# Optimization experiments

Hardware: AMD Instinct MI355X
Metric: run time of the kernel (lower is better)

The kernel has to match this reference:

```python
import jax, jax.numpy as jnp
import numpy as np

N, E, G = 10000, 160000, 64      # nodes, edges, graphs
IN, H, L = 128, 128, 14          # in_channels, hidden, num GENConv layers
EPS_LN = 1e-5                    # torch LayerNorm eps
EPS_MSG = 1e-7                   # GENConv message eps


def layer_norm(x, g, b):
    mu = jnp.mean(x, axis=-1, keepdims=True)
    v = jnp.var(x, axis=-1, keepdims=True)
    return (x - mu) * jax.lax.rsqrt(v + EPS_LN) * g + b


def gen_conv(h, src, dst, t, sc, W1, b1, mg, mb, W2, b2):
    # message: relu(x_j) + eps  (no edge_attr)
    msg = jax.nn.relu(h[src]) + EPS_MSG                      # [E, H]
    # softmax aggregation over edges sharing a destination, per feature
    z = msg * t
    mx = jax.ops.segment_max(z, dst, num_segments=N)         # [N, H]
    mx = jnp.where(jnp.isfinite(mx), mx, 0.0)
    e = jnp.exp(z - mx[dst])
    ssum = jax.ops.segment_sum(e, dst, num_segments=N)
    alpha = e / (ssum[dst] + 1e-16)
    agg = jax.ops.segment_sum(msg * alpha, dst, num_segments=N)  # [N, H]
    # MessageNorm: normalize(agg) * ||h|| * scale
    agg = agg / jnp.maximum(jnp.linalg.norm(agg, axis=-1, keepdims=True), 1e-12)
    agg = agg * jnp.linalg.norm(h, axis=-1, keepdims=True) * sc
    out = h + agg
    # MLP [H, 2H, H] with LayerNorm + ReLU between (dropout off in eval)
    z1 = layer_norm(out @ W1 + b1, mg, mb)
    return jax.nn.relu(z1) @ W2 + b2


def setup_inputs() -> dict:
    key = jax.random.key(0)
    ks = jax.random.split(key, 8)
    s = 0.05
    x = jax.random.normal(ks[0], (N, IN), jnp.float32)
    edge_index = jax.random.randint(ks[1], (2, E), 0, N, dtype=jnp.int64)
    batch = jnp.sort(jax.random.randint(ks[2], (N,), 0, G, dtype=jnp.int64))
    enc_W = jax.random.normal(ks[3], (IN, H), jnp.float32) * s
    enc_b = jnp.zeros((H,), jnp.float32)
    ln_g = jnp.ones((L, H), jnp.float32)
    ln_b = jnp.zeros((L, H), jnp.float32)
    t = jnp.ones((L,), jnp.float32)         # learnable softmax temperature
    scale = jnp.ones((L,), jnp.float32)     # learnable MsgNorm scale
    W1 = jax.random.normal(ks[4], (L, H, 2 * H), jnp.float32) * s
    b1 = jnp.zeros((L, 2 * H), jnp.float32)
    mg = jnp.ones((L, 2 * H), jnp.float32)
    mb = jnp.zeros((L, 2 * H), jnp.float32)
    W2 = jax.random.normal(ks[5], (L, 2 * H, H), jnp.float32) * s
    b2 = jnp.zeros((L, H), jnp.float32)
    fn_g = jnp.ones((H,), jnp.float32)
    fn_b = jnp.zeros((H,), jnp.float32)
    return dict(x=x, edge_index=edge_index, batch=batch, enc_W=enc_W, enc_b=enc_b,
                ln_g=ln_g, ln_b=ln_b, t=t, scale=scale, W1=W1, b1=b1, mg=mg, mb=mb,
                W2=W2, b2=b2, fn_g=fn_g, fn_b=fn_b)


def reference(x, edge_index, batch, enc_W, enc_b, ln_g, ln_b, t, scale,
              W1, b1, mg, mb, W2, b2, fn_g, fn_b):
    src, dst = edge_index[0], edge_index[1]
    h = x @ enc_W + enc_b
    for i in range(L):  # DeepGCNLayer 'res+': x + conv(act(norm(x)))
        r = jax.nn.leaky_relu(layer_norm(h, ln_g[i], ln_b[i]), 0.01)
        h = h + gen_conv(r, src, dst, t[i], scale[i],
                         W1[i], b1[i], mg[i], mb[i], W2[i], b2[i])
    h = jax.nn.leaky_relu(layer_norm(h, fn_g, fn_b), 0.01)
    # global_mean_pool (fin_map is unused in the original forward)
    cnt = jax.ops.segment_sum(jnp.ones((N,), h.dtype), batch, num_segments=G)
    gf = jax.ops.segment_sum(h, batch, num_segments=G) / jnp.maximum(cnt, 1.0)[:, None]
    return gf
```

## Files before the change

### kernel.cpp

```cpp
#include <hip/hip_runtime.h>
#include <cstdint>
#include <cstddef>


#define BT 512

typedef __attribute__((ext_vector_type(8))) short bf16x8;
typedef __attribute__((ext_vector_type(4))) float f32x4;

__device__ inline float bf2f(ushort u) {
    union { uint i; float f; } v;
    v.i = (uint)u << 16;
    return v.f;
}
__device__ inline ushort f2bf(float f) {
    union { float f; uint i; } v;
    v.f = f;
    return (ushort)((v.i + 0x7fffu + ((v.i >> 16) & 1u)) >> 16);
}
__device__ inline uint f2bf2(float a, float b) {
    return (uint)f2bf(a) | ((uint)f2bf(b) << 16);
}
__device__ inline float fast_exp2(float x) {
    return __builtin_amdgcn_exp2f(x);
}

__global__ void setup_kernel(const float* __restrict__ x, ushort* __restrict__ xb,
                             const int* __restrict__ dst, int* __restrict__ deg,
                             const int* __restrict__ batch, int* __restrict__ gstart,
                             int total, int N, int E, int G) {
    int idx = blockIdx.x * blockDim.x + threadIdx.x;
    if (idx >= total) return;
    xb[idx] = f2bf(x[idx]);
    if (idx < E) atomicAdd(&deg[dst[idx]], 1);
    if (idx < N) {
        int bb = batch[idx];
        if (idx == 0)
            for (int g = 0; g <= bb; g++) gstart[g] = 0;
        else {
            int pb = batch[idx - 1];
            for (int g = pb + 1; g <= bb; g++) gstart[g] = idx;
        }
        if (idx == N - 1)
            for (int g = bb + 1; g <= G; g++) gstart[g] = N;
    }
}

__global__ __launch_bounds__(1024) void scan_kernel(const int* __restrict__ deg,
                                                    int* __restrict__ offs,
                                                    int* __restrict__ cursor, int N) {
    __shared__ int part[1024];
    int tid = threadIdx.x;
    int CH = (N + 1023) / 1024;
    int base = tid * CH;
    int s = 0;
    for (int i = 0; i < CH; i++) {
        int idx = base + i;
        if (idx < N) s += deg[idx];
    }
    part[tid] = s;
    __syncthreads();
    for (int off = 1; off < 1024; off <<= 1) {
        int v = (tid >= off) ? part[tid - off] : 0;
        __syncthreads();
        part[tid] += v;
        __syncthreads();
    }
    int run = (tid == 0) ? 0 : part[tid - 1];
    for (int i = 0; i < CH; i++) {
        int idx = base + i;
        if (idx < N) {
            offs[idx] = run;
            cursor[idx] = run;
            run += deg[idx];
        }
    }
    if (tid == 1023) offs[N] = part[1023];
}

__global__ void scatter_kernel(const int* __restrict__ src, const int* __restrict__ dst,
                               int* __restrict__ cursor, int* __restrict__ esrc, int E) {
    int e = blockIdx.x * blockDim.x + threadIdx.x;
    if (e < E) {
        int d = dst[e];
        int pos = atomicAdd(&cursor[d], 1);
        esrc[pos] = src[e];
    }
}

__global__ __launch_bounds__(1024) void sort_kernel(const int* __restrict__ offs,
                                                    int* __restrict__ perm, int N) {
    __shared__ int hist[256];
    __shared__ int cur[256];
    int tid = threadIdx.x;
    if (tid < 256) hist[tid] = 0;
    __syncthreads();
    for (int n = tid; n < N; n += 1024) {
        int d = offs[n + 1] - offs[n];
        int key = 255 - min(d, 255);
        atomicAdd(&hist[key], 1);
    }
    __syncthreads();
    if (tid == 0) {
        int run = 0;
        for (int i = 0; i < 256; i++) {
            cur[i] = run;
            run += hist[i];
        }
    }
    __syncthreads();
    for (int n = tid; n < N; n += 1024) {
        int d = offs[n + 1] - offs[n];
        int key = 255 - min(d, 255);
        int pos = atomicAdd(&cur[key], 1);
        perm[pos] = n;
    }
}

__global__ __launch_bounds__(256) void prep_kernel(const float* __restrict__ W1,
                                                   const float* __restrict__ W2,
                                                   const float* __restrict__ encW,
                                                   ushort* __restrict__ W1t,
                                                   ushort* __restrict__ W2t,
                                                   ushort* __restrict__ encWt, int L) {
    __shared__ float tile[32][33];
    int z = blockIdx.z;
    const float* in;
    ushort* out;
    int R, C;
    if (z < L) {
        in = W1 + (size_t)z * 32768; out = W1t + (size_t)z * 32768; R = 128; C = 256;
    } else if (z < 2 * L) {
        int i = z - L;
        in = W2 + (size_t)i * 32768; out = W2t + (size_t)i * 32768; R = 256; C = 128;
    } else {
        in = encW; out = encWt; R = 128; C = 128;
    }
    int r0 = blockIdx.y * 32, c0 = blockIdx.x * 32;
    if (r0 >= R || c0 >= C) return;
    int tx = threadIdx.x & 31, ty = threadIdx.x >> 5;
    for (int i = ty; i < 32; i += 8) tile[i][tx] = in[(size_t)(r0 + i) * C + c0 + tx];
    __syncthreads();
    for (int i = ty; i < 32; i += 8)
        out[(size_t)(c0 + i) * R + r0 + tx] = f2bf(tile[tx][i]);
}

__device__ __forceinline__ void agg_stage(const ushort* __restrict__ rin,
                                          const int* __restrict__ offs,
                                          const int* __restrict__ esrc,
                                          const float* __restrict__ rnbuf,
                                          float tv2, float sv,
                                          int nd0, int nd1,
                                          int w, int l, uint (*AsU)[68]) {
    const uint2* rin2 = (const uint2*)rin;
    int half = l >> 5, li = l & 31;
    int eb[2], dg[2];
    eb[0] = offs[nd0]; dg[0] = offs[nd0 + 1] - eb[0];
    eb[1] = offs[nd1]; dg[1] = offs[nd1 + 1] - eb[1];

    uint2 ru0 = rin2[(size_t)nd0 * 32 + li];
    uint2 ru1 = rin2[(size_t)nd1 * 32 + li];
    float rn0 = rnbuf[nd0], rn1 = rnbuf[nd1];

    float s[2][4] = {}, W[2][4] = {};
    int mxdeg = max(dg[0], dg[1]);

#pragma unroll 1
    for (int base = 0; base < mxdeg; base += 64) {
        int rem0 = min(dg[0] - base, 64);
        int rem1 = min(dg[1] - base, 64);
        int idx0 = (rem0 > 0 && l < rem0) ? esrc[eb[0] + base + l] : 0;
        int idx1 = (rem1 > 0 && l < rem1) ? esrc[eb[1] + base + l] : 0;
        int it = (max(rem0, rem1) + 7) >> 3;
#pragma unroll 1
        for (int i = 0; i < it; i++) {
            int j0 = i * 8 + half;
            uint2 rv[2][4];
            bool vl[2][4];
#pragma unroll
            for (int c = 0; c < 4; c++) {
                int j = j0 + 2 * c;
                vl[0][c] = j < rem0;
                vl[1][c] = j < rem1;
                int sn0 = __shfl(idx0, j, 64);
                int sn1 = __shfl(idx1, j, 64);
                if (vl[0][c]) rv[0][c] = rin2[(size_t)sn0 * 32 + li];
                if (vl[1][c]) rv[1][c] = rin2[(size_t)sn1 * 32 + li];
            }
#pragma unroll
            for (int k = 0; k < 2; k++)
#pragma unroll
                for (int c = 0; c < 4; c++) {
                    if (vl[k][c]) {
                        float f0 = bf2f((ushort)(rv[k][c].x & 0xffff));
                        float f1 = bf2f((ushort)(rv[k][c].x >> 16));
                        float f2 = bf2f((ushort)(rv[k][c].y & 0xffff));
                        float f3 = bf2f((ushort)(rv[k][c].y >> 16));
                        float g0 = fmaxf(f0, 0.f) + 1e-7f;
                        float g1 = fmaxf(f1, 0.f) + 1e-7f;
                        float g2 = fmaxf(f2, 0.f) + 1e-7f;
                        float g3 = fmaxf(f3, 0.f) + 1e-7f;
                        float p0 = fast_exp2(g0 * tv2);
                        float p1 = fast_exp2(g1 * tv2);
                        float p2 = fast_exp2(g2 * tv2);
                        float p3 = fast_exp2(g3 * tv2);
                        s[k][0] += p0; W[k][0] += g0 * p0;
                        s[k][1] += p1; W[k][1] += g1 * p1;
                        s[k][2] += p2; W[k][2] += g2 * p2;
                        s[k][3] += p3; W[k][3] += g3 * p3;
                    }
                }
        }
    }

#pragma unroll
    for (int k = 0; k < 2; k++) {
#pragma unroll
        for (int f = 0; f < 4; f++) {
            s[k][f] += __shfl_xor(s[k][f], 32, 64);
            W[k][f] += __shfl_xor(W[k][f], 32, 64);
        }
        float agg[4], nsq = 0.f;
#pragma unroll
        for (int f = 0; f < 4; f++) {
            agg[f] = W[k][f] / (s[k][f] + 1e-16f);
            nsq += agg[f] * agg[f];
        }
#pragma unroll
        for (int off = 1; off < 32; off <<= 1) nsq += __shfl_xor(nsq, off, 64);
        float rnv = (k == 0) ? rn0 : rn1;
        uint2 ru = (k == 0) ? ru0 : ru1;
        float fac = rnv * sv / fmaxf(sqrtf(nsq), 1e-12f);
        if (half == 0) {
            uint2 o;
            o.x = f2bf2(bf2f((ushort)(ru.x & 0xffff)) + agg[0] * fac,
                        bf2f((ushort)(ru.x >> 16)) + agg[1] * fac);
            o.y = f2bf2(bf2f((ushort)(ru.y & 0xffff)) + agg[2] * fac,
                        bf2f((ushort)(ru.y >> 16)) + agg[3] * fac);
            *(uint2*)&AsU[2 * w + k][2 * li] = o;
        }
    }
}

__device__ __forceinline__ void gemm1_stage8(const ushort (*As)[136],
                                             const ushort* __restrict__ Bt,
                                             const float* __restrict__ bias,
                                             const float* __restrict__ mg,
                                             const float* __restrict__ mb,
                                             ushort (*z1s)[264],
                                             int w, int q, int ln,
                                             float (*pS)[16], float (*pQ)[16]) {
    f32x4 acc[2];
    acc[0] = (f32x4){0.f, 0.f, 0.f, 0.f};
    acc[1] = (f32x4){0.f, 0.f, 0.f, 0.f};
#pragma unroll
    for (int ks = 0; ks < 128; ks += 32) {
        bf16x8 a = *(const bf16x8*)&As[ln][ks + q * 8];
#pragma unroll
        for (int ct = 0; ct < 2; ct++) {
            bf16x8 bv = *(const bf16x8*)(Bt + (size_t)(w * 32 + ct * 16 + ln) * 128 + ks + q * 8);
            acc[ct] = __builtin_amdgcn_mfma_f32_16x16x32_bf16(a, bv, acc[ct], 0, 0, 0);
        }
    }
    float s1[4] = {0, 0, 0, 0}, s2[4] = {0, 0, 0, 0};
#pragma unroll
    for (int ct = 0; ct < 2; ct++)
#pragma unroll
        for (int r = 0; r < 4; r++) {
            float v = acc[ct][r] + bias[w * 32 + ct * 16 + ln];
            acc[ct][r] = v;
            s1[r] += v;
            s2[r] += v * v;
        }
#pragma unroll
    for (int off = 1; off < 16; off <<= 1)
#pragma unroll
        for (int r = 0; r < 4; r++) {
            s1[r] += __shfl_xor(s1[r], off, 64);
            s2[r] += __shfl_xor(s2[r], off, 64);
        }
    if (ln == 0)
#pragma unroll
        for (int r = 0; r < 4; r++) {
            pS[w][q * 4 + r] = s1[r];
            pQ[w][q * 4 + r] = s2[r];
        }
    __syncthreads();
#pragma unroll
    for (int r = 0; r < 4; r++) {
        int row = q * 4 + r;
        float S = 0.f, Q = 0.f;
#pragma unroll
        for (int ww = 0; ww < 8; ww++) {
            S += pS[ww][row];
            Q += pQ[ww][row];
        }
        float mu = S * (1.f / 256.f);
        float var = Q * (1.f / 256.f) - mu * mu;
        float rs = rsqrtf(var + 1e-5f);
#pragma unroll
        for (int ct = 0; ct < 2; ct++) {
            int col = w * 32 + ct * 16 + ln;
            float y = (acc[ct][r] - mu) * rs * mg[col] + mb[col];
            z1s[row][col] = f2bf(fmaxf(y, 0.f));
        }
    }
    __syncthreads();
}

template <int KD, bool RESID>
__device__ __forceinline__ void out_stage8(const ushort* __restrict__ Abase, int astr,
                                           const ushort* __restrict__ Bt,
                                           const float* __restrict__ bias,
                                           const float* __restrict__ lg,
                                           const float* __restrict__ lb,
                                           ushort* __restrict__ hbuf,
                                           ushort* __restrict__ rout,
                                           float* __restrict__ rnbuf,
                                           const int* rowmap,
                                           int w, int q, int ln,
                                           float (*pS)[16], float (*pQ)[16]) {
    f32x4 acc = (f32x4){0.f, 0.f, 0.f, 0.f};
    int col = w * 16 + ln;
#pragma unroll
    for (int ks = 0; ks < KD; ks += 32) {
        bf16x8 a = *(const bf16x8*)(Abase + ln * astr + ks + q * 8);
        bf16x8 bv = *(const bf16x8*)(Bt + (size_t)col * KD + ks + q * 8);
        acc = __builtin_amdgcn_mfma_f32_16x16x32_bf16(a, bv, acc, 0, 0, 0);
    }
    float s1[4], s2[4];
#pragma unroll
    for (int r = 0; r < 4; r++) {
        int grow = rowmap[q * 4 + r];
        float v = acc[r] + bias[col];
        if (RESID) v += bf2f(__builtin_nontemporal_load(hbuf + (size_t)grow * 128 + col));
        __builtin_nontemporal_store(f2bf(v), hbuf + (size_t)grow * 128 + col);
        acc[r] = v;
        s1[r] = v;
        s2[r] = v * v;
    }
#pragma unroll
    for (int off = 1; off < 16; off <<= 1)
#pragma unroll
        for (int r = 0; r < 4; r++) {
            s1[r] += __shfl_xor(s1[r], off, 64);
            s2[r] += __shfl_xor(s2[r], off, 64);
        }
    if (ln == 0)
#pragma unroll
        for (int r = 0; r < 4; r++) {
            pS[w][q * 4 + r] = s1[r];
            pQ[w][q * 4 + r] = s2[r];
        }
    __syncthreads();
    float yv[4];
    float t2[4];
#pragma unroll
    for (int r = 0; r < 4; r++) {
        int row = q * 4 + r;
        float S = 0.f, Q = 0.f;
#pragma unroll
        for (int ww = 0; ww < 8; ww++) {
            S += pS[ww][row];
            Q += pQ[ww][row];
        }
        float mu = S * (1.f / 128.f);
        float var = Q * (1.f / 128.f) - mu * mu;
        float rs = rsqrtf(var + 1e-5f);
        float y = (acc[r] - mu) * rs * lg[col] + lb[col];
        y = y > 0.f ? y : 0.01f * y;
        yv[r] = y;
        t2[r] = y * y;
    }
#pragma unroll
    for (int off = 1; off < 16; off <<= 1)
#pragma unroll
        for (int r = 0; r < 4; r++) t2[r] += __shfl_xor(t2[r], off, 64);
    __syncthreads();
    if (ln == 0)
#pragma unroll
        for (int r = 0; r < 4; r++) pS[w][q * 4 + r] = t2[r];
    __syncthreads();
#pragma unroll
    for (int r = 0; r < 4; r++) {
        int grow = rowmap[q * 4 + r];
        float T = 0.f;
#pragma unroll
        for (int ww = 0; ww < 8; ww++) T += pS[ww][q * 4 + r];
        if (w == 0 && ln == 0) rnbuf[grow] = sqrtf(T);
        __builtin_nontemporal_store(f2bf(yv[r]), rout + (size_t)grow * 128 + col);
    }
}

__global__ __launch_bounds__(BT, 4) void enc_kernel(const ushort* __restrict__ xb,
                                                    const ushort* __restrict__ encWt,
                                                    const float* __restrict__ encB,
                                                    const float* __restrict__ lg,
                                                    const float* __restrict__ lb,
                                                    ushort* __restrict__ h,
                                                    ushort* __restrict__ rbuf,
                                                    float* __restrict__ rn, int N) {
    __shared__ __align__(16) ushort As[16][136];
    __shared__ float pS[8][16], pQ[8][16];
    __shared__ int rowmap[16];
    uint(*AsU)[68] = (uint(*)[68])As;
    int tid = threadIdx.x, w = tid >> 6, l = tid & 63;
    int q = l >> 4, ln = l & 15;
    int row0 = blockIdx.x * 16;
    if (tid < 16) rowmap[tid] = row0 + tid;
    for (int idx = tid; idx < 16 * 64; idx += BT) {
        int row = idx >> 6, cl = idx & 63;
        AsU[row][cl] =
            __builtin_nontemporal_load(((const uint*)xb) + (size_t)(row0 + row) * 64 + cl);
    }
    __syncthreads();
    out_stage8<128, false>(&As[0][0], 136, encWt, encB, lg, lb, h, rbuf, rn,
                           rowmap, w, q, ln, pS, pQ);
}

__global__ __launch_bounds__(BT, 4) void layer_kernel(const ushort* __restrict__ rin,
                                                      ushort* __restrict__ rout,
                                                      const int* __restrict__ offs,
                                                      const int* __restrict__ esrc,
                                                      const int* __restrict__ perm,
                                                      float* __restrict__ rn,
                                                      ushort* __restrict__ h,
                                                      const ushort* __restrict__ W1t,
                                                      const ushort* __restrict__ W2t,
                                                      const float* __restrict__ b1,
                                                      const float* __restrict__ mg,
                                                      const float* __restrict__ mb,
                                                      const float* __restrict__ b2,
                                                      const float* __restrict__ ng,
                                                      const float* __restrict__ nb,
                                                      const float* __restrict__ tptr,
                                                      const float* __restrict__ scptr,
                                                      int N) {
    __shared__ __align__(16) ushort As[16][136];
    __shared__ __align__(16) ushort z1s[16][264];
    __shared__ float pS[8][16], pQ[8][16];
    __shared__ int rowmap[16];
    uint(*AsU)[68] = (uint(*)[68])As;
    int tid = threadIdx.x, w = tid >> 6, l = tid & 63;
    int q = l >> 4, ln = l & 15;
    int row0 = blockIdx.x * 16;
    if (tid < 16) rowmap[tid] = perm[row0 + tid];
    __syncthreads();
    float tv2 = (*tptr) * 1.4426950408889634f;
    float sv = *scptr;
    agg_stage(rin, offs, esrc, rn, tv2, sv,
              rowmap[2 * w], rowmap[2 * w + 1], w, l, AsU);
    __syncthreads();
    gemm1_stage8(As, W1t, b1, mg, mb, z1s, w, q, ln, pS, pQ);
    out_stage8<256, true>(&z1s[0][0], 264, W2t, b2, ng, nb, h, rout, rn,
                          rowmap, w, q, ln, pS, pQ);
}

__global__ __launch_bounds__(256) void pool_kernel(const ushort* __restrict__ rf,
                                                   const int* __restrict__ gstart,
                                                   float* __restrict__ out) {
    __shared__ float pb0[4][64], pb1[4][64];
    int g = blockIdx.x;
    int w = threadIdx.x >> 6, l = threadIdx.x & 63;
    int s = gstart[g], e = gstart[g + 1];
    float a0 = 0.f, a1 = 0.f;
    for (int n = s + w; n < e; n += 4) {
        uint rv = __builtin_nontemporal_load(((const uint*)rf) + (size_t)n * 64 + l);
        a0 += bf2f((ushort)(rv & 0xffff));
        a1 += bf2f((ushort)(rv >> 16));
    }
    pb0[w][l] = a0;
    pb1[w][l] = a1;
    __syncthreads();
    if (threadIdx.x < 64) {
        float t0 = pb0[0][l] + pb0[1][l] + pb0[2][l] + pb0[3][l];
        float t1 = pb1[0][l] + pb1[1][l] + pb1[2][l] + pb1[3][l];
        float inv = 1.f / fmaxf((float)(e - s), 1.f);
        out[g * 128 + 2 * l] = t0 * inv;
        out[g * 128 + 2 * l + 1] = t1 * inv;
    }
}

extern "C" void kernel_launch(void* const* d_in, const int* in_sizes, int n_in,
                              void* d_out, int out_size, void* d_ws, size_t ws_size,
                              hipStream_t stream) {
    const float* x     = (const float*)d_in[0];
    const int*   ei    = (const int*)d_in[1];
    const int*   batch = (const int*)d_in[2];
    const float* encW  = (const float*)d_in[3];
    const float* encB  = (const float*)d_in[4];
    const float* ln_g  = (const float*)d_in[5];
    const float* ln_b  = (const float*)d_in[6];
    const float* tArr  = (const float*)d_in[7];
    const float* scArr = (const float*)d_in[8];
    const float* W1    = (const float*)d_in[9];
    const float* b1    = (const float*)d_in[10];
    const float* mg    = (const float*)d_in[11];
    const float* mb    = (const float*)d_in[12];
    const float* W2    = (const float*)d_in[13];
    const float* b2    = (const float*)d_in[14];
    const float* fn_g  = (const float*)d_in[15];
    const float* fn_b  = (const float*)d_in[16];
    float* out = (float*)d_out;

    const int N = in_sizes[0] / 128;
    const int E = in_sizes[1] / 2;
    const int L = in_sizes[7];
    const int G = 64;

    const int* src = ei;
    const int* dst = ei + E;

    char* p = (char*)d_ws;
    auto alloc = [&](size_t bytes) -> void* {
        void* qp = (void*)p;
        p += (bytes + 255) & ~(size_t)255;
        return qp;
    };
    int*    deg    = (int*)alloc((size_t)N * 4);
    int*    offs   = (int*)alloc((size_t)(N + 1) * 4);
    int*    cursor = (int*)alloc((size_t)N * 4);
    int*    esrc   = (int*)alloc((size_t)E * 4);
    int*    gstart = (int*)alloc((size_t)(G + 1) * 4);
    int*    perm   = (int*)alloc((size_t)N * 4);
    ushort* h      = (ushort*)alloc((size_t)N * 128 * 2);
    ushort* r0     = (ushort*)alloc((size_t)N * 128 * 2);
    ushort* r1     = (ushort*)alloc((size_t)N * 128 * 2);
    float*  rn     = (float*)alloc((size_t)N * 4);
    ushort* xb     = (ushort*)alloc((size_t)N * 128 * 2);
    ushort* W1t    = (ushort*)alloc((size_t)L * 32768 * 2);
    ushort* W2t    = (ushort*)alloc((size_t)L * 32768 * 2);
    ushort* encWt  = (ushort*)alloc((size_t)16384 * 2);

    (void)hipMemsetAsync(deg, 0, (size_t)N * 4, stream);

    setup_kernel<<<(N * 128 + 255) / 256, 256, 0, stream>>>(x, xb, dst, deg, batch,
                                                            gstart, N * 128, N, E, G);
    scan_kernel<<<1, 1024, 0, stream>>>(deg, offs, cursor, N);
    scatter_kernel<<<(E + 255) / 256, 256, 0, stream>>>(src, dst, cursor, esrc, E);
    sort_kernel<<<1, 1024, 0, stream>>>(offs, perm, N);
    prep_kernel<<<dim3(8, 8, 2 * L + 1), 256, 0, stream>>>(W1, W2, encW, W1t, W2t,
                                                           encWt, L);

    const int TILES = N / 16;

    enc_kernel<<<TILES, BT, 0, stream>>>(xb, encWt, encB, ln_g, ln_b, h, r0, rn, N);

    for (int i = 0; i < L; i++) {
        const ushort* rin = (i & 1) ? r1 : r0;
        ushort* rout = (i & 1) ? r0 : r1;
        const float* ng = (i < L - 1) ? (ln_g + (size_t)(i + 1) * 128) : fn_g;
        const float* nb = (i < L - 1) ? (ln_b + (size_t)(i + 1) * 128) : fn_b;
        layer_kernel<<<TILES, BT, 0, stream>>>(rin, rout, offs, esrc, perm, rn, h,
                                               W1t + ((size_t)i << 15),
                                               W2t + ((size_t)i << 15),
                                               b1 + (size_t)i * 256,
                                               mg + (size_t)i * 256,
                                               mb + (size_t)i * 256,
                                               b2 + (size_t)i * 128,
                                               ng, nb, tArr + i, scArr + i, N);
    }

    const ushort* rf = ((L - 1) & 1) ? r0 : r1;
    pool_kernel<<<G, 256, 0, stream>>>(rf, gstart, out);
}
```

Baseline: 572.4 us.

## Fuse encoder, all layers and pooling into one persistent kernel with grid barriers

```diff
diff --git a/kernel.cpp b/kernel.cpp
--- a/kernel.cpp
+++ b/kernel.cpp
@@ -4,6 +4,7 @@
 
 
 #define BT 512
+#define NBLK 512
 
 typedef __attribute__((ext_vector_type(8))) short bf16x8;
 typedef __attribute__((ext_vector_type(4))) float f32x4;
@@ -23,6 +24,23 @@
 }
 __device__ inline float fast_exp2(float x) {
     return __builtin_amdgcn_exp2f(x);
+}
+
+__device__ __forceinline__ void gbar(uint* __restrict__ bar, uint nb) {
+    __syncthreads();
+    if (threadIdx.x == 0) {
+        uint g = __hip_atomic_load(bar + 1, __ATOMIC_RELAXED, __HIP_MEMORY_SCOPE_AGENT);
+        uint v = __hip_atomic_fetch_add(bar + 0, 1u, __ATOMIC_ACQ_REL, __HIP_MEMORY_SCOPE_AGENT);
+        if (v == nb - 1u) {
+            __hip_atomic_store(bar + 0, 0u, __ATOMIC_RELAXED, __HIP_MEMORY_SCOPE_AGENT);
+            __hip_atomic_fetch_add(bar + 1, 1u, __ATOMIC_RELEASE, __HIP_MEMORY_SCOPE_AGENT);
+        } else {
+            while (__hip_atomic_load(bar + 1, __ATOMIC_RELAXED, __HIP_MEMORY_SCOPE_AGENT) == g)
+                __builtin_amdgcn_s_sleep(4);
+            __threadfence();
+        }
+    }
+    __syncthreads();
 }
 
 __global__ void setup_kernel(const float* __restrict__ x, ushort* __restrict__ xb,
@@ -392,50 +410,33 @@
     }
 }
 
-__global__ __launch_bounds__(BT, 4) void enc_kernel(const ushort* __restrict__ xb,
-                                                    const ushort* __restrict__ encWt,
-                                                    const float* __restrict__ encB,
-                                                    const float* __restrict__ lg,
-                                                    const float* __restrict__ lb,
-                                                    ushort* __restrict__ h,
-                                                    ushort* __restrict__ rbuf,
-                                                    float* __restrict__ rn, int N) {
-    __shared__ __align__(16) ushort As[16][136];
-    __shared__ float pS[8][16], pQ[8][16];
-    __shared__ int rowmap[16];
-    uint(*AsU)[68] = (uint(*)[68])As;
-    int tid = threadIdx.x, w = tid >> 6, l = tid & 63;
-    int q = l >> 4, ln = l & 15;
-    int row0 = blockIdx.x * 16;
-    if (tid < 16) rowmap[tid] = row0 + tid;
-    for (int idx = tid; idx < 16 * 64; idx += BT) {
-        int row = idx >> 6, cl = idx & 63;
-        AsU[row][cl] =
-            __builtin_nontemporal_load(((const uint*)xb) + (size_t)(row0 + row) * 64 + cl);
-    }
-    __syncthreads();
-    out_stage8<128, false>(&As[0][0], 136, encWt, encB, lg, lb, h, rbuf, rn,
-                           rowmap, w, q, ln, pS, pQ);
-}
-
-__global__ __launch_bounds__(BT, 4) void layer_kernel(const ushort* __restrict__ rin,
-                                                      ushort* __restrict__ rout,
-                                                      const int* __restrict__ offs,
-                                                      const int* __restrict__ esrc,
-                                                      const int* __restrict__ perm,
-                                                      float* __restrict__ rn,
-                                                      ushort* __restrict__ h,
-                                                      const ushort* __restrict__ W1t,
-                                                      const ushort* __restrict__ W2t,
-                                                      const float* __restrict__ b1,
-                                                      const float* __restrict__ mg,
-                                                      const float* __restrict__ mb,
-                                                      const float* __restrict__ b2,
-                                                      const float* __restrict__ ng,
-                                                      const float* __restrict__ nb,
-                                                      const float* __restrict__ tptr,
-                                                      const float* __restrict__ scptr,
-                                                      int N) {
+__global__ __launch_bounds__(BT, 4) void fused_kernel(
+    const ushort* __restrict__ xb,
+    const ushort* __restrict__ encWt,
+    const float* __restrict__ encB,
+    const float* __restrict__ ln_g,
+    const float* __restrict__ ln_b,
+    const float* __restrict__ fn_g,
+    const float* __restrict__ fn_b,
+    const float* __restrict__ tArr,
+    const float* __restrict__ scArr,
+    const ushort* __restrict__ W1t,
+    const ushort* __restrict__ W2t,
+    const float* __restrict__ b1,
+    const float* __restrict__ mg,
+    const float* __restrict__ mb,
+    const float* __restrict__ b2,
+    const int* __restrict__ offs,
+    const int* __restrict__ esrc,
+    const int* __restrict__ perm,
+    float* __restrict__ rn,
+    ushort* __restrict__ h,
+    ushort* __restrict__ r0,
+    ushort* __restrict__ r1,
+    const int* __restrict__ gstart,
+    float* __restrict__ out,
+    uint* __restrict__ bar,
+    int N, int L, int G) {
     __shared__ __align__(16) ushort As[16][136];
     __shared__ __align__(16) ushort z1s[16][264];
     __shared__ float pS[8][16], pQ[8][16];
@@ -443,41 +444,95 @@
     uint(*AsU)[68] = (uint(*)[68])As;
     int tid = threadIdx.x, w = tid >> 6, l = tid & 63;
     int q = l >> 4, ln = l & 15;
-    int row0 = blockIdx.x * 16;
-    if (tid < 16) rowmap[tid] = perm[row0 + tid];
-    __syncthreads();
-    float tv2 = (*tptr) * 1.4426950408889634f;
-    float sv = *scptr;
-    agg_stage(rin, offs, esrc, rn, tv2, sv,
-              rowmap[2 * w], rowmap[2 * w + 1], w, l, AsU);
-    __syncthreads();
-    gemm1_stage8(As, W1t, b1, mg, mb, z1s, w, q, ln, pS, pQ);
-    out_stage8<256, true>(&z1s[0][0], 264, W2t, b2, ng, nb, h, rout, rn,
-                          rowmap, w, q, ln, pS, pQ);
-}
-
-__global__ __launch_bounds__(256) void pool_kernel(const ushort* __restrict__ rf,
-                                                   const int* __restrict__ gstart,
-                                                   float* __restrict__ out) {
-    __shared__ float pb0[4][64], pb1[4][64];
-    int g = blockIdx.x;
-    int w = threadIdx.x >> 6, l = threadIdx.x & 63;
-    int s = gstart[g], e = gstart[g + 1];
-    float a0 = 0.f, a1 = 0.f;
-    for (int n = s + w; n < e; n += 4) {
-        uint rv = __builtin_nontemporal_load(((const uint*)rf) + (size_t)n * 64 + l);
-        a0 += bf2f((ushort)(rv & 0xffff));
-        a1 += bf2f((ushort)(rv >> 16));
-    }
-    pb0[w][l] = a0;
-    pb1[w][l] = a1;
-    __syncthreads();
-    if (threadIdx.x < 64) {
-        float t0 = pb0[0][l] + pb0[1][l] + pb0[2][l] + pb0[3][l];
-        float t1 = pb1[0][l] + pb1[1][l] + pb1[2][l] + pb1[3][l];
-        float inv = 1.f / fmaxf((float)(e - s), 1.f);
-        out[g * 128 + 2 * l] = t0 * inv;
-        out[g * 128 + 2 * l + 1] = t1 * inv;
+    int bid = blockIdx.x;
+    const int NB = (int)gridDim.x;
+    const int TILES = N / 16;
+
+    int singles = 2 * NB - TILES;
+    int t0, t1;
+    if (bid < singles) {
+        t0 = bid; t1 = -1;
+    } else {
+        int k = bid - singles;
+        t0 = singles + 2 * k;
+        t1 = t0 + 1;
+    }
+    if (t0 >= TILES) t0 = -1;
+    if (t1 >= TILES) t1 = -1;
+
+    for (int ii = 0; ii < 2; ii++) {
+        int t = ii ? t1 : t0;
+        if (t < 0) continue;
+        int row0 = t * 16;
+        if (tid < 16) rowmap[tid] = row0 + tid;
+        for (int idx = tid; idx < 16 * 64; idx += BT) {
+            int rr = idx >> 6, cl = idx & 63;
+            AsU[rr][cl] = __builtin_nontemporal_load(
+                ((const uint*)xb) + (size_t)(row0 + rr) * 64 + cl);
+        }
+        __syncthreads();
+        out_stage8<128, false>(&As[0][0], 136, encWt, encB, ln_g, ln_b, h, r0, rn,
+                               rowmap, w, q, ln, pS, pQ);
+        __syncthreads();
+    }
+    gbar(bar, (uint)NB);
+
+    for (int i = 0; i < L; i++) {
+        const ushort* rin = (i & 1) ? r1 : r0;
+        ushort* rout = (i & 1) ? r0 : r1;
+        const float* ng = (i < L - 1) ? (ln_g + (size_t)(i + 1) * 128) : fn_g;
+        const float* nbv = (i < L - 1) ? (ln_b + (size_t)(i + 1) * 128) : fn_b;
+        const ushort* w1 = W1t + ((size_t)i << 15);
+        const ushort* w2 = W2t + ((size_t)i << 15);
+        const float* b1i = b1 + (size_t)i * 256;
+        const float* mgi = mg + (size_t)i * 256;
+        const float* mbi = mb + (size_t)i * 256;
+        const float* b2i = b2 + (size_t)i * 128;
+        float tv2 = tArr[i] * 1.4426950408889634f;
+        float sv = scArr[i];
+        for (int ii = 0; ii < 2; ii++) {
+            int t = ii ? t1 : t0;
+            if (t < 0) continue;
+            int row0 = t * 16;
+            if (tid < 16) rowmap[tid] = perm[row0 + tid];
+            __syncthreads();
+            agg_stage(rin, offs, esrc, rn, tv2, sv,
+                      rowmap[2 * w], rowmap[2 * w + 1], w, l, AsU);
+            __syncthreads();
+            gemm1_stage8(As, w1, b1i, mgi, mbi, z1s, w, q, ln, pS, pQ);
+            out_stage8<256, true>(&z1s[0][0], 264, w2, b2i, ng, nbv, h, rout, rn,
+                                  rowmap, w, q, ln, pS, pQ);
+            __syncthreads();
+        }
+        gbar(bar, (uint)NB);
+    }
+
+    if (bid < G) {
+        const ushort* rf = ((L - 1) & 1) ? r0 : r1;
+        float* pb0 = (float*)&z1s[0][0];
+        float* pb1 = pb0 + 8 * 64;
+        int g = bid;
+        int s = gstart[g], e = gstart[g + 1];
+        float a0 = 0.f, a1 = 0.f;
+        for (int n = s + w; n < e; n += 8) {
+            uint rv = ((const uint*)rf)[(size_t)n * 64 + l];
+            a0 += bf2f((ushort)(rv & 0xffff));
+            a1 += bf2f((ushort)(rv >> 16));
+        }
+        pb0[w * 64 + l] = a0;
+        pb1[w * 64 + l] = a1;
+        __syncthreads();
+        if (tid < 64) {
+            float s0 = 0.f, s1 = 0.f;
+#pragma unroll
+            for (int ww = 0; ww < 8; ww++) {
+                s0 += pb0[ww * 64 + tid];
+                s1 += pb1[ww * 64 + tid];
+            }
+            float inv = 1.f / fmaxf((float)(e - s), 1.f);
+            out[g * 128 + 2 * tid] = s0 * inv;
+            out[g * 128 + 2 * tid + 1] = s1 * inv;
+        }
     }
 }
 
@@ -531,8 +586,10 @@
     ushort* W1t    = (ushort*)alloc((size_t)L * 32768 * 2);
     ushort* W2t    = (ushort*)alloc((size_t)L * 32768 * 2);
     ushort* encWt  = (ushort*)alloc((size_t)16384 * 2);
+    uint*   bar    = (uint*)alloc(256);
 
     (void)hipMemsetAsync(deg, 0, (size_t)N * 4, stream);
+    (void)hipMemsetAsync(bar, 0, 256, stream);
 
     setup_kernel<<<(N * 128 + 255) / 256, 256, 0, stream>>>(x, xb, dst, deg, batch,
                                                             gstart, N * 128, N, E, G);
@@ -542,25 +599,8 @@
     prep_kernel<<<dim3(8, 8, 2 * L + 1), 256, 0, stream>>>(W1, W2, encW, W1t, W2t,
                                                            encWt, L);
 
-    const int TILES = N / 16;
-
-    enc_kernel<<<TILES, BT, 0, stream>>>(xb, encWt, encB, ln_g, ln_b, h, r0, rn, N);
-
-    for (int i = 0; i < L; i++) {
-        const ushort* rin = (i & 1) ? r1 : r0;
-        ushort* rout = (i & 1) ? r0 : r1;
-        const float* ng = (i < L - 1) ? (ln_g + (size_t)(i + 1) * 128) : fn_g;
-        const float* nb = (i < L - 1) ? (ln_b + (size_t)(i + 1) * 128) : fn_b;
-        layer_kernel<<<TILES, BT, 0, stream>>>(rin, rout, offs, esrc, perm, rn, h,
-                                               W1t + ((size_t)i << 15),
-                                               W2t + ((size_t)i << 15),
-                                               b1 + (size_t)i * 256,
-                                               mg + (size_t)i * 256,
-                                               mb + (size_t)i * 256,
-                                               b2 + (size_t)i * 128,
-                                               ng, nb, tArr + i, scArr + i, N);
-    }
-
-    const ushort* rf = ((L - 1) & 1) ? r0 : r1;
-    pool_kernel<<<G, 256, 0, stream>>>(rf, gstart, out);
-}
+    fused_kernel<<<NBLK, BT, 0, stream>>>(xb, encWt, encB, ln_g, ln_b, fn_g, fn_b,
+                                          tArr, scArr, W1t, W2t, b1, mg, mb, b2,
+                                          offs, esrc, perm, rn, h, r0, r1,
+                                          gstart, out, bar, N, L, G);
+}
```

Result: slower. 1.643 ms (+187.1%).

## Halve block size to 256 threads and process 8 rows per block

Applied to the files above, without the earlier changes.

```diff
diff --git a/kernel.cpp b/kernel.cpp
--- a/kernel.cpp
+++ b/kernel.cpp
@@ -3,7 +3,7 @@
 #include <cstddef>
 
 
-#define BT 512
+#define BT 256
 
 typedef __attribute__((ext_vector_type(8))) short bf16x8;
 typedef __attribute__((ext_vector_type(4))) float f32x4;
@@ -242,7 +242,7 @@
     }
 }
 
-__device__ __forceinline__ void gemm1_stage8(const ushort (*As)[136],
+__device__ __forceinline__ void gemm1_stage4(const ushort (*As)[136],
                                              const ushort* __restrict__ Bt,
                                              const float* __restrict__ bias,
                                              const float* __restrict__ mg,
@@ -250,24 +250,24 @@
                                              ushort (*z1s)[264],
                                              int w, int q, int ln,
                                              float (*pS)[16], float (*pQ)[16]) {
-    f32x4 acc[2];
-    acc[0] = (f32x4){0.f, 0.f, 0.f, 0.f};
-    acc[1] = (f32x4){0.f, 0.f, 0.f, 0.f};
+    f32x4 acc[4];
+#pragma unroll
+    for (int ct = 0; ct < 4; ct++) acc[ct] = (f32x4){0.f, 0.f, 0.f, 0.f};
 #pragma unroll
     for (int ks = 0; ks < 128; ks += 32) {
         bf16x8 a = *(const bf16x8*)&As[ln][ks + q * 8];
 #pragma unroll
-        for (int ct = 0; ct < 2; ct++) {
-            bf16x8 bv = *(const bf16x8*)(Bt + (size_t)(w * 32 + ct * 16 + ln) * 128 + ks + q * 8);
+        for (int ct = 0; ct < 4; ct++) {
+            bf16x8 bv = *(const bf16x8*)(Bt + (size_t)(w * 64 + ct * 16 + ln) * 128 + ks + q * 8);
             acc[ct] = __builtin_amdgcn_mfma_f32_16x16x32_bf16(a, bv, acc[ct], 0, 0, 0);
         }
     }
     float s1[4] = {0, 0, 0, 0}, s2[4] = {0, 0, 0, 0};
 #pragma unroll
-    for (int ct = 0; ct < 2; ct++)
+    for (int ct = 0; ct < 4; ct++)
 #pragma unroll
         for (int r = 0; r < 4; r++) {
-            float v = acc[ct][r] + bias[w * 32 + ct * 16 + ln];
+            float v = acc[ct][r] + bias[w * 64 + ct * 16 + ln];
             acc[ct][r] = v;
             s1[r] += v;
             s2[r] += v * v;
@@ -291,7 +291,7 @@
         int row = q * 4 + r;
         float S = 0.f, Q = 0.f;
 #pragma unroll
-        for (int ww = 0; ww < 8; ww++) {
+        for (int ww = 0; ww < 4; ww++) {
             S += pS[ww][row];
             Q += pQ[ww][row];
         }
@@ -299,8 +299,8 @@
         float var = Q * (1.f / 256.f) - mu * mu;
         float rs = rsqrtf(var + 1e-5f);
 #pragma unroll
-        for (int ct = 0; ct < 2; ct++) {
-            int col = w * 32 + ct * 16 + ln;
+        for (int ct = 0; ct < 4; ct++) {
+            int col = w * 64 + ct * 16 + ln;
             float y = (acc[ct][r] - mu) * rs * mg[col] + mb[col];
             z1s[row][col] = f2bf(fmaxf(y, 0.f));
         }
@@ -309,7 +309,7 @@
 }
 
 template <int KD, bool RESID>
-__device__ __forceinline__ void out_stage8(const ushort* __restrict__ Abase, int astr,
+__device__ __forceinline__ void out_stage4(const ushort* __restrict__ Abase, int astr,
                                            const ushort* __restrict__ Bt,
                                            const float* __restrict__ bias,
                                            const float* __restrict__ lg,
@@ -320,24 +320,36 @@
                                            const int* rowmap,
                                            int w, int q, int ln,
                                            float (*pS)[16], float (*pQ)[16]) {
-    f32x4 acc = (f32x4){0.f, 0.f, 0.f, 0.f};
-    int col = w * 16 + ln;
+    f32x4 acc[2];
+    acc[0] = (f32x4){0.f, 0.f, 0.f, 0.f};
+    acc[1] = (f32x4){0.f, 0.f, 0.f, 0.f};
+    int col0 = w * 32 + ln;
+    int col1 = w * 32 + 16 + ln;
 #pragma unroll
     for (int ks = 0; ks < KD; ks += 32) {
         bf16x8 a = *(const bf16x8*)(Abase + ln * astr + ks + q * 8);
-        bf16x8 bv = *(const bf16x8*)(Bt + (size_t)col * KD + ks + q * 8);
-        acc = __builtin_amdgcn_mfma_f32_16x16x32_bf16(a, bv, acc, 0, 0, 0);
-    }
-    float s1[4], s2[4];
+        bf16x8 b0 = *(const bf16x8*)(Bt + (size_t)col0 * KD + ks + q * 8);
+        bf16x8 b1v = *(const bf16x8*)(Bt + (size_t)col1 * KD + ks + q * 8);
+        acc[0] = __builtin_amdgcn_mfma_f32_16x16x32_bf16(a, b0, acc[0], 0, 0, 0);
+        acc[1] = __builtin_amdgcn_mfma_f32_16x16x32_bf16(a, b1v, acc[1], 0, 0, 0);
+    }
+    float v0[4], v1[4], s1[4], s2[4];
 #pragma unroll
     for (int r = 0; r < 4; r++) {
-        int grow = rowmap[q * 4 + r];
-        float v = acc[r] + bias[col];
-        if (RESID) v += bf2f(__builtin_nontemporal_load(hbuf + (size_t)grow * 128 + col));
-        __builtin_nontemporal_store(f2bf(v), hbuf + (size_t)grow * 128 + col);
-        acc[r] = v;
-        s1[r] = v;
-        s2[r] = v * v;
+        int row = q * 4 + r;
+        int grow = rowmap[row];
+        v0[r] = acc[0][r] + bias[col0];
+        v1[r] = acc[1][r] + bias[col1];
+        if (row < 8) {
+            if (RESID) {
+                v0[r] += bf2f(__builtin_nontemporal_load(hbuf + (size_t)grow * 128 + col0));
+                v1[r] += bf2f(__builtin_nontemporal_load(hbuf + (size_t)grow * 128 + col1));
+            }
+            __builtin_nontemporal_store(f2bf(v0[r]), hbuf + (size_t)grow * 128 + col0);
+            __builtin_nontemporal_store(f2bf(v1[r]), hbuf + (size_t)grow * 128 + col1);
+        }
+        s1[r] = v0[r] + v1[r];
+        s2[r] = v0[r] * v0[r] + v1[r] * v1[r];
     }
 #pragma unroll
     for (int off = 1; off < 16; off <<= 1)
@@ -353,24 +365,26 @@
             pQ[w][q * 4 + r] = s2[r];
         }
     __syncthreads();
-    float yv[4];
-    float t2[4];
+    float y0[4], y1[4], t2[4];
 #pragma unroll
     for (int r = 0; r < 4; r++) {
         int row = q * 4 + r;
         float S = 0.f, Q = 0.f;
 #pragma unroll
-        for (int ww = 0; ww < 8; ww++) {
+        for (int ww = 0; ww < 4; ww++) {
             S += pS[ww][row];
             Q += pQ[ww][row];
         }
         float mu = S * (1.f / 128.f);
         float var = Q * (1.f / 128.f) - mu * mu;
         float rs = rsqrtf(var + 1e-5f);
-        float y = (acc[r] - mu) * rs * lg[col] + lb[col];
-        y = y > 0.f ? y : 0.01f * y;
-        yv[r] = y;
-        t2[r] = y * y;
+        float a0 = (v0[r] - mu) * rs * lg[col0] + lb[col0];
+        float a1 = (v1[r] - mu) * rs * lg[col1] + lb[col1];
+        a0 = a0 > 0.f ? a0 : 0.01f * a0;
+        a1 = a1 > 0.f ? a1 : 0.01f * a1;
+        y0[r] = a0;
+        y1[r] = a1;
+        t2[r] = a0 * a0 + a1 * a1;
     }
 #pragma unroll
     for (int off = 1; off < 16; off <<= 1)
@@ -383,16 +397,20 @@
     __syncthreads();
 #pragma unroll
     for (int r = 0; r < 4; r++) {
-        int grow = rowmap[q * 4 + r];
-        float T = 0.f;
-#pragma unroll
-        for (int ww = 0; ww < 8; ww++) T += pS[ww][q * 4 + r];
-        if (w == 0 && ln == 0) rnbuf[grow] = sqrtf(T);
-        __builtin_nontemporal_store(f2bf(yv[r]), rout + (size_t)grow * 128 + col);
-    }
-}
-
-__global__ __launch_bounds__(BT, 4) void enc_kernel(const ushort* __restrict__ xb,
+        int row = q * 4 + r;
+        if (row < 8) {
+            int grow = rowmap[row];
+            float T = 0.f;
+#pragma unroll
+            for (int ww = 0; ww < 4; ww++) T += pS[ww][row];
+            if (w == 0 && ln == 0) rnbuf[grow] = sqrtf(T);
+            __builtin_nontemporal_store(f2bf(y0[r]), rout + (size_t)grow * 128 + col0);
+            __builtin_nontemporal_store(f2bf(y1[r]), rout + (size_t)grow * 128 + col1);
+        }
+    }
+}
+
+__global__ __launch_bounds__(BT, 6) void enc_kernel(const ushort* __restrict__ xb,
                                                     const ushort* __restrict__ encWt,
                                                     const float* __restrict__ encB,
                                                     const float* __restrict__ lg,
@@ -401,24 +419,24 @@
                                                     ushort* __restrict__ rbuf,
                                                     float* __restrict__ rn, int N) {
     __shared__ __align__(16) ushort As[16][136];
-    __shared__ float pS[8][16], pQ[8][16];
+    __shared__ float pS[4][16], pQ[4][16];
     __shared__ int rowmap[16];
     uint(*AsU)[68] = (uint(*)[68])As;
     int tid = threadIdx.x, w = tid >> 6, l = tid & 63;
     int q = l >> 4, ln = l & 15;
-    int row0 = blockIdx.x * 16;
-    if (tid < 16) rowmap[tid] = row0 + tid;
-    for (int idx = tid; idx < 16 * 64; idx += BT) {
+    int row0 = blockIdx.x * 8;
+    if (tid < 16) rowmap[tid] = row0 + (tid & 7);
+    for (int idx = tid; idx < 8 * 64; idx += BT) {
         int row = idx >> 6, cl = idx & 63;
         AsU[row][cl] =
             __builtin_nontemporal_load(((const uint*)xb) + (size_t)(row0 + row) * 64 + cl);
     }
     __syncthreads();
-    out_stage8<128, false>(&As[0][0], 136, encWt, encB, lg, lb, h, rbuf, rn,
+    out_stage4<128, false>(&As[0][0], 136, encWt, encB, lg, lb, h, rbuf, rn,
                            rowmap, w, q, ln, pS, pQ);
 }
 
-__global__ __launch_bounds__(BT, 4) void layer_kernel(const ushort* __restrict__ rin,
+__global__ __launch_bounds__(BT, 6) void layer_kernel(const ushort* __restrict__ rin,
                                                       ushort* __restrict__ rout,
                                                       const int* __restrict__ offs,
                                                       const int* __restrict__ esrc,
@@ -438,21 +456,21 @@
                                                       int N) {
     __shared__ __align__(16) ushort As[16][136];
     __shared__ __align__(16) ushort z1s[16][264];
-    __shared__ float pS[8][16], pQ[8][16];
+    __shared__ float pS[4][16], pQ[4][16];
     __shared__ int rowmap[16];
     uint(*AsU)[68] = (uint(*)[68])As;
     int tid = threadIdx.x, w = tid >> 6, l = tid & 63;
     int q = l >> 4, ln = l & 15;
-    int row0 = blockIdx.x * 16;
-    if (tid < 16) rowmap[tid] = perm[row0 + tid];
+    int row0 = blockIdx.x * 8;
+    if (tid < 16) rowmap[tid] = perm[row0 + (tid & 7)];
     __syncthreads();
     float tv2 = (*tptr) * 1.4426950408889634f;
     float sv = *scptr;
     agg_stage(rin, offs, esrc, rn, tv2, sv,
               rowmap[2 * w], rowmap[2 * w + 1], w, l, AsU);
     __syncthreads();
-    gemm1_stage8(As, W1t, b1, mg, mb, z1s, w, q, ln, pS, pQ);
-    out_stage8<256, true>(&z1s[0][0], 264, W2t, b2, ng, nb, h, rout, rn,
+    gemm1_stage4(As, W1t, b1, mg, mb, z1s, w, q, ln, pS, pQ);
+    out_stage4<256, true>(&z1s[0][0], 264, W2t, b2, ng, nb, h, rout, rn,
                           rowmap, w, q, ln, pS, pQ);
 }
 
@@ -542,7 +560,7 @@
     prep_kernel<<<dim3(8, 8, 2 * L + 1), 256, 0, stream>>>(W1, W2, encW, W1t, W2t,
                                                            encWt, L);
 
-    const int TILES = N / 16;
+    const int TILES = N / 8;
 
     enc_kernel<<<TILES, BT, 0, stream>>>(xb, encWt, encB, ln_g, ln_b, h, r0, rn, N);
 
```

After: 637.4 us. 1.11x slower.
